# Kernel tuning notes

Measured on AMD Instinct MI355X. Metric: run time of the kernel, lower is better.

Reference implementation:

```python
import jax, jax.numpy as jnp
import numpy as np

N_NODES = 100000
N_EDGES = 1600000
F_IN, H1, H2, N_CLASSES = 512, 64, 32, 16


def setup_inputs() -> dict:
    key = jax.random.key(0)
    ks = jax.random.split(key, 8)
    glorot = lambda k, fi, fo: jax.random.normal(k, (fi, fo), jnp.float32) * (2.0 / (fi + fo)) ** 0.5
    return {
        "x": jax.random.normal(ks[0], (N_NODES, F_IN), jnp.float32),
        "edge_index": jax.random.randint(ks[1], (2, N_EDGES), 0, N_NODES, jnp.int32),
        "W1": glorot(ks[2], F_IN, H1), "b1": jnp.zeros((H1,), jnp.float32),
        "W2": glorot(ks[3], H1, H2), "b2": jnp.zeros((H2,), jnp.float32),
        "W3": glorot(ks[4], H2, N_CLASSES), "b3": jnp.zeros((N_CLASSES,), jnp.float32),
    }


def _gcn_conv(x, W, b, src, dst, norm, n_nodes):
    # GCNConv: D^{-1/2} (A + I) D^{-1/2} X W + b  (transform-then-propagate)
    h = x @ W                                   # [N, out]
    msg = h[src] * norm[:, None]                # gather + scale, [E', out]
    agg = jax.ops.segment_sum(msg, dst, num_segments=n_nodes)  # scatter-add
    return agg + b


def reference(x, edge_index, W1, b1, W2, b2, W3, b3):
    n = x.shape[0]
    loop = jnp.arange(n, dtype=edge_index.dtype)
    src = jnp.concatenate([edge_index[0], loop])  # add self-loops
    dst = jnp.concatenate([edge_index[1], loop])
    deg = jax.ops.segment_sum(jnp.ones_like(src, dtype=x.dtype), dst, num_segments=n)
    dinv = jnp.where(deg > 0, jax.lax.rsqrt(deg), 0.0)
    norm = dinv[src] * dinv[dst]                  # symmetric normalization per edge

    h = jax.nn.relu(_gcn_conv(x, W1, b1, src, dst, norm, n))
    h = jax.nn.relu(_gcn_conv(h, W2, b2, src, dst, norm, n))  # dropout = identity (eval)
    h = _gcn_conv(h, W3, b3, src, dst, norm, n)
    return jax.nn.log_softmax(h, axis=1)
```

## Files before the change

kernel.cpp:

```cpp
#include <hip/hip_runtime.h>
#include <hip/hip_bf16.h>
#include <cstdint>
#include <cstddef>

#define N_NODES 100000
#define N_EDGES 1600000
#define F_IN 512
#define H1F 64
#define H2F 32
#define NCF 16

typedef __attribute__((ext_vector_type(8))) short bf16x8;
typedef __attribute__((ext_vector_type(4))) float f32x4;

__device__ inline short f2bf(float f) {
    uint32_t u = __builtin_bit_cast(uint32_t, f);
    return (short)((u + 0x7FFF + ((u >> 16) & 1)) >> 16);
}

__global__ __launch_bounds__(256) void hist_kernel(const int* __restrict__ dst,
                                                   int* __restrict__ cnt) {
    int e = blockIdx.x * 256 + threadIdx.x;
    if (e < N_EDGES) atomicAdd(&cnt[dst[e]], 1);
}

__global__ __launch_bounds__(512) void scanA_kernel(const int* __restrict__ cnt,
                                                    int* __restrict__ bsums) {
    __shared__ int sh[8];
    int i = blockIdx.x * 512 + threadIdx.x;
    int v = (i < N_NODES) ? cnt[i] : 0;
    #pragma unroll
    for (int o = 32; o > 0; o >>= 1) v += __shfl_down(v, o);
    if ((threadIdx.x & 63) == 0) sh[threadIdx.x >> 6] = v;
    __syncthreads();
    if (threadIdx.x == 0) {
        int t = 0;
        #pragma unroll
        for (int w = 0; w < 8; ++w) t += sh[w];
        bsums[blockIdx.x] = t;
    }
}

__global__ __launch_bounds__(256) void scanB_kernel(int* __restrict__ bsums, int n) {
    __shared__ int s[256];
    int t = threadIdx.x;
    int v = (t < n) ? bsums[t] : 0;
    s[t] = v;
    __syncthreads();
    for (int o = 1; o < 256; o <<= 1) {
        int a = (t >= o) ? s[t - o] : 0;
        __syncthreads();
        s[t] += a;
        __syncthreads();
    }
    if (t < n) bsums[t] = s[t] - v;
}

__global__ __launch_bounds__(512) void scanC_kernel(const int* __restrict__ cnt,
                                                    const int* __restrict__ bsums,
                                                    int* __restrict__ row_ptr,
                                                    int* __restrict__ cursor) {
    __shared__ int s[512];
    int t = threadIdx.x;
    int i = blockIdx.x * 512 + t;
    int v = (i < N_NODES) ? cnt[i] : 0;
    s[t] = v;
    __syncthreads();
    for (int o = 1; o < 512; o <<= 1) {
        int a = (t >= o) ? s[t - o] : 0;
        __syncthreads();
        s[t] += a;
        __syncthreads();
    }
    if (i < N_NODES) {
        int ex = s[t] - v + bsums[blockIdx.x];
        row_ptr[i] = ex;
        cursor[i]  = ex;
    }
    if (i == N_NODES - 1) row_ptr[N_NODES] = s[t] + bsums[blockIdx.x];
}

__global__ __launch_bounds__(256) void dinv_kernel(const int* __restrict__ cnt,
                                                   float* __restrict__ dinv) {
    int i = blockIdx.x * 256 + threadIdx.x;
    if (i < N_NODES) dinv[i] = rsqrtf((float)(cnt[i] + 1));
}

__global__ __launch_bounds__(256) void scatter_kernel(const int* __restrict__ src,
                                                      const int* __restrict__ dst,
                                                      int* __restrict__ cursor,
                                                      int* __restrict__ col) {
    int e = blockIdx.x * 256 + threadIdx.x;
    if (e < N_EDGES) {
        int d = dst[e];
        int pos = atomicAdd(&cursor[d], 1);
        col[pos] = src[e];
    }
}

__global__ __launch_bounds__(256) void gemm1_mfma(const float* __restrict__ x,
                                                  const float* __restrict__ W,
                                                  const float* __restrict__ dinv,
                                                  float* __restrict__ out) {
    __shared__ short As[2][4096];
    __shared__ short Bs[2][2048];
    const int tid = threadIdx.x;
    const int L = tid & 63;
    const int w = tid >> 6;
    const int brow = blockIdx.x * 128;

    f32x4 acc[2][4] = {};

    auto stageA = [&](int kt, int buf) {
        #pragma unroll
        for (int h = 0; h < 2; ++h) {
            int r  = (tid >> 2) + h * 64;
            int kg = tid & 3;
            int gr = brow + r;
            float4 v0 = make_float4(0.f, 0.f, 0.f, 0.f);
            float4 v1 = make_float4(0.f, 0.f, 0.f, 0.f);
            if (gr < N_NODES) {
                const float* p = &x[(size_t)gr * F_IN + kt * 32 + kg * 8];
                v0 = *reinterpret_cast<const float4*>(p);
                v1 = *reinterpret_cast<const float4*>(p + 4);
            }
            short t8[8] = {f2bf(v0.x), f2bf(v0.y), f2bf(v0.z), f2bf(v0.w),
                           f2bf(v1.x), f2bf(v1.y), f2bf(v1.z), f2bf(v1.w)};
            *reinterpret_cast<bf16x8*>(&As[buf][kg * 1024 + (r ^ (kg << 2)) * 8]) =
                *reinterpret_cast<bf16x8*>(t8);
        }
    };
    auto stageB = [&](int kt, int buf) {
        int k0 = kt * 32 + w * 8;
        short t8[8];
        #pragma unroll
        for (int i = 0; i < 8; ++i) t8[i] = f2bf(W[(size_t)(k0 + i) * H1F + L]);
        int byteoff = L * 64 + ((w * 16) ^ ((L & 3) << 4));
        *reinterpret_cast<bf16x8*>((char*)Bs[buf] + byteoff) =
            *reinterpret_cast<bf16x8*>(t8);
    };
    auto compute = [&](int buf) {
        const int kg = L >> 4;
        const int lr = L & 15;
        int r0 = w * 32 + lr;
        int r1 = r0 + 16;
        bf16x8 a0 = *reinterpret_cast<bf16x8*>(&As[buf][kg * 1024 + (r0 ^ (kg << 2)) * 8]);
        bf16x8 a1 = *reinterpret_cast<bf16x8*>(&As[buf][kg * 1024 + (r1 ^ (kg << 2)) * 8]);
        #pragma unroll
        for (int ni = 0; ni < 4; ++ni) {
            int c = ni * 16 + lr;
            bf16x8 b = *reinterpret_cast<bf16x8*>(
                (char*)Bs[buf] + c * 64 + ((kg * 16) ^ ((c & 3) << 4)));
            acc[0][ni] = __builtin_amdgcn_mfma_f32_16x16x32_bf16(a0, b, acc[0][ni], 0, 0, 0);
            acc[1][ni] = __builtin_amdgcn_mfma_f32_16x16x32_bf16(a1, b, acc[1][ni], 0, 0, 0);
        }
    };

    stageA(0, 0);
    stageB(0, 0);
    __syncthreads();
    for (int kt = 0; kt < 16; ++kt) {
        int cur = kt & 1;
        if (kt < 15) {
            stageA(kt + 1, cur ^ 1);
            stageB(kt + 1, cur ^ 1);
        }
        compute(cur);
        __syncthreads();
    }

    #pragma unroll
    for (int mi = 0; mi < 2; ++mi) {
        #pragma unroll
        for (int i = 0; i < 4; ++i) {
            int row = brow + w * 32 + mi * 16 + (L >> 4) * 4 + i;
            if (row < N_NODES) {
                float dv = dinv[row];
                #pragma unroll
                for (int ni = 0; ni < 4; ++ni)
                    out[(size_t)row * H1F + ni * 16 + (L & 15)] = acc[mi][ni][i] * dv;
            }
        }
    }
}

__global__ __launch_bounds__(256) void gemm2_kernel(const float* __restrict__ h,
                                                    const float* __restrict__ W,
                                                    const float* __restrict__ dinv,
                                                    float* __restrict__ out) {
    __shared__ float ws[64][32];
    __shared__ float rs[8][64];
    int tid = threadIdx.x;
    int brow = blockIdx.x * 8;
    #pragma unroll
    for (int i = 0; i < 2; ++i) {
        int f = tid + i * 256;
        reinterpret_cast<float4*>(&ws[0][0])[f] = reinterpret_cast<const float4*>(W)[f];
    }
    if (tid < 128) {
        float4 v = reinterpret_cast<const float4*>(h)[(size_t)brow * 16 + tid];
        reinterpret_cast<float4*>(&rs[0][0])[tid] = v;
    }
    __syncthreads();
    int lr = tid >> 5;
    int c = tid & 31;
    float acc = 0.f;
    #pragma unroll
    for (int k = 0; k < 64; ++k) acc += rs[lr][k] * ws[k][c];
    int gr = brow + lr;
    out[(size_t)gr * H2F + c] = acc * dinv[gr];
}

__global__ __launch_bounds__(256) void gemm3_kernel(const float* __restrict__ h,
                                                    const float* __restrict__ W,
                                                    const float* __restrict__ dinv,
                                                    float* __restrict__ out) {
    __shared__ float ws[32][16];
    __shared__ float rs[16][32];
    int tid = threadIdx.x;
    int brow = blockIdx.x * 16;
    if (tid < 128) {
        reinterpret_cast<float4*>(&ws[0][0])[tid] = reinterpret_cast<const float4*>(W)[tid];
    } else {
        int t = tid - 128;
        float4 v = reinterpret_cast<const float4*>(h)[(size_t)brow * 8 + t];
        reinterpret_cast<float4*>(&rs[0][0])[t] = v;
    }
    __syncthreads();
    int lr = tid >> 4;
    int c = tid & 15;
    float acc = 0.f;
    #pragma unroll
    for (int k = 0; k < 32; ++k) acc += rs[lr][k] * ws[k][c];
    int gr = brow + lr;
    out[(size_t)gr * NCF + c] = acc * dinv[gr];
}

template <int F, bool RELU, bool LSM>
__global__ __launch_bounds__(256) void aggregate_kernel(const float* __restrict__ h,
                                                        const int* __restrict__ row_ptr,
                                                        const int* __restrict__ col,
                                                        const float* __restrict__ dinv,
                                                        const float* __restrict__ bias,
                                                        float* __restrict__ out) {
    int tid = blockIdx.x * 256 + threadIdx.x;
    int n = tid / F;
    int f = tid % F;
    if (n >= N_NODES) return;
    int beg = row_ptr[n];
    int end = row_ptr[n + 1];
    float sum = h[(size_t)n * F + f];
    int j = beg;
    for (; j + 3 < end; j += 4) {
        int c0 = col[j], c1 = col[j + 1], c2 = col[j + 2], c3 = col[j + 3];
        float s0 = h[(size_t)c0 * F + f];
        float s1 = h[(size_t)c1 * F + f];
        float s2 = h[(size_t)c2 * F + f];
        float s3 = h[(size_t)c3 * F + f];
        sum += (s0 + s1) + (s2 + s3);
    }
    for (; j < end; ++j) sum += h[(size_t)col[j] * F + f];

    float val = sum * dinv[n] + bias[f];
    if (RELU) val = fmaxf(val, 0.f);
    if (LSM) {
        float m = val;
        #pragma unroll
        for (int o = 1; o < F; o <<= 1) m = fmaxf(m, __shfl_xor(m, o));
        float ex = expf(val - m);
        float s = ex;
        #pragma unroll
        for (int o = 1; o < F; o <<= 1) s += __shfl_xor(s, o);
        val = val - m - logf(s);
    }
    out[(size_t)n * F + f] = val;
}

extern "C" void kernel_launch(void* const* d_in, const int* in_sizes, int n_in,
                              void* d_out, int out_size, void* d_ws, size_t ws_size,
                              hipStream_t stream) {
    const float* x  = (const float*)d_in[0];
    const int*   ei = (const int*)d_in[1];
    const float* W1 = (const float*)d_in[2];
    const float* b1 = (const float*)d_in[3];
    const float* W2 = (const float*)d_in[4];
    const float* b2 = (const float*)d_in[5];
    const float* W3 = (const float*)d_in[6];
    const float* b3 = (const float*)d_in[7];
    float* out = (float*)d_out;

    const int* src = ei;
    const int* dst = ei + N_EDGES;

    char* ws = (char*)d_ws;
    size_t off = 0;
    auto alloc = [&](size_t bytes) -> void* {
        void* p = ws + off;
        off += (bytes + 255) & ~(size_t)255;
        return p;
    };
    int*   cnt     = (int*)alloc((size_t)N_NODES * 4);
    int*   row_ptr = (int*)alloc((size_t)(N_NODES + 1) * 4);
    int*   cursor  = (int*)alloc((size_t)N_NODES * 4);
    int*   bsums   = (int*)alloc(1024);
    float* dinv    = (float*)alloc((size_t)N_NODES * 4);
    int*   col     = (int*)alloc((size_t)N_EDGES * 4);
    float* bufA    = (float*)alloc((size_t)N_NODES * 64 * 4);
    float* bufB    = (float*)alloc((size_t)N_NODES * 64 * 4);

    const int nChunks = (N_NODES + 511) / 512;

    hipMemsetAsync(cnt, 0, (size_t)N_NODES * 4, stream);
    hist_kernel<<<(N_EDGES + 255) / 256, 256, 0, stream>>>(dst, cnt);
    scanA_kernel<<<nChunks, 512, 0, stream>>>(cnt, bsums);
    scanB_kernel<<<1, 256, 0, stream>>>(bsums, nChunks);
    scanC_kernel<<<nChunks, 512, 0, stream>>>(cnt, bsums, row_ptr, cursor);
    dinv_kernel<<<(N_NODES + 255) / 256, 256, 0, stream>>>(cnt, dinv);
    scatter_kernel<<<(N_EDGES + 255) / 256, 256, 0, stream>>>(src, dst, cursor, col);

    gemm1_mfma<<<(N_NODES + 127) / 128, 256, 0, stream>>>(x, W1, dinv, bufA);
    aggregate_kernel<64, true, false><<<(N_NODES * 64) / 256, 256, 0, stream>>>(
        bufA, row_ptr, col, dinv, b1, bufB);

    gemm2_kernel<<<N_NODES / 8, 256, 0, stream>>>(bufB, W2, dinv, bufA);
    aggregate_kernel<32, true, false><<<(N_NODES * 32) / 256, 256, 0, stream>>>(
        bufA, row_ptr, col, dinv, b2, bufB);

    gemm3_kernel<<<N_NODES / 16, 256, 0, stream>>>(bufB, W3, dinv, bufA);
    aggregate_kernel<16, false, true><<<(N_NODES * 16) / 256, 256, 0, stream>>>(
        bufA, row_ptr, col, dinv, b3, out);
}
```

Baseline: 667.9 us.

## Build CSR via two-level bucketed counting sort with shared-memory histograms

Replaces the per-node global-atomic histogram, three-kernel scan and per-node scatter with a two-level bucketed sort. Edges are first histogrammed and scattered into 782 buckets of 128 destination nodes, with the local node index packed into high bits of the source id. A per-bucket kernel then computes node counts, row_ptr, dinv and the final col ordering using shared-memory atomics. This cuts global atomic contention and the number of launches, at the cost of an extra pass over an intermediate edge buffer that reuses bufA.

```diff
diff --git a/kernel.cpp b/kernel.cpp
--- a/kernel.cpp
+++ b/kernel.cpp
@@ -9,6 +9,7 @@
 #define H1F 64
 #define H2F 32
 #define NCF 16
+#define NB 782
 
 typedef __attribute__((ext_vector_type(8))) short bf16x8;
 typedef __attribute__((ext_vector_type(4))) float f32x4;
@@ -18,83 +19,97 @@
     return (short)((u + 0x7FFF + ((u >> 16) & 1)) >> 16);
 }
 
-__global__ __launch_bounds__(256) void hist_kernel(const int* __restrict__ dst,
-                                                   int* __restrict__ cnt) {
-    int e = blockIdx.x * 256 + threadIdx.x;
-    if (e < N_EDGES) atomicAdd(&cnt[dst[e]], 1);
-}
-
-__global__ __launch_bounds__(512) void scanA_kernel(const int* __restrict__ cnt,
-                                                    int* __restrict__ bsums) {
-    __shared__ int sh[8];
-    int i = blockIdx.x * 512 + threadIdx.x;
-    int v = (i < N_NODES) ? cnt[i] : 0;
-    #pragma unroll
-    for (int o = 32; o > 0; o >>= 1) v += __shfl_down(v, o);
-    if ((threadIdx.x & 63) == 0) sh[threadIdx.x >> 6] = v;
-    __syncthreads();
-    if (threadIdx.x == 0) {
-        int t = 0;
-        #pragma unroll
-        for (int w = 0; w < 8; ++w) t += sh[w];
-        bsums[blockIdx.x] = t;
-    }
-}
-
-__global__ __launch_bounds__(256) void scanB_kernel(int* __restrict__ bsums, int n) {
-    __shared__ int s[256];
+__global__ __launch_bounds__(256) void bhist_kernel(const int* __restrict__ dst,
+                                                    int* __restrict__ bcnt) {
+    __shared__ int lh[NB];
+    for (int i = threadIdx.x; i < NB; i += 256) lh[i] = 0;
+    __syncthreads();
+    for (int e = blockIdx.x * 256 + threadIdx.x; e < N_EDGES; e += 256 * 256)
+        atomicAdd(&lh[dst[e] >> 7], 1);
+    __syncthreads();
+    for (int i = threadIdx.x; i < NB; i += 256) {
+        int v = lh[i];
+        if (v) atomicAdd(&bcnt[i], v);
+    }
+}
+
+__global__ __launch_bounds__(1024) void bscan_kernel(const int* __restrict__ bcnt,
+                                                     int* __restrict__ boff,
+                                                     int* __restrict__ bcur,
+                                                     int* __restrict__ row_ptr) {
+    __shared__ int s[1024];
     int t = threadIdx.x;
-    int v = (t < n) ? bsums[t] : 0;
+    int v = (t < NB) ? bcnt[t] : 0;
     s[t] = v;
     __syncthreads();
-    for (int o = 1; o < 256; o <<= 1) {
+    for (int o = 1; o < 1024; o <<= 1) {
         int a = (t >= o) ? s[t - o] : 0;
         __syncthreads();
         s[t] += a;
         __syncthreads();
     }
-    if (t < n) bsums[t] = s[t] - v;
-}
-
-__global__ __launch_bounds__(512) void scanC_kernel(const int* __restrict__ cnt,
-                                                    const int* __restrict__ bsums,
-                                                    int* __restrict__ row_ptr,
-                                                    int* __restrict__ cursor) {
-    __shared__ int s[512];
-    int t = threadIdx.x;
-    int i = blockIdx.x * 512 + t;
-    int v = (i < N_NODES) ? cnt[i] : 0;
-    s[t] = v;
-    __syncthreads();
-    for (int o = 1; o < 512; o <<= 1) {
-        int a = (t >= o) ? s[t - o] : 0;
-        __syncthreads();
-        s[t] += a;
-        __syncthreads();
-    }
-    if (i < N_NODES) {
-        int ex = s[t] - v + bsums[blockIdx.x];
-        row_ptr[i] = ex;
-        cursor[i]  = ex;
-    }
-    if (i == N_NODES - 1) row_ptr[N_NODES] = s[t] + bsums[blockIdx.x];
-}
-
-__global__ __launch_bounds__(256) void dinv_kernel(const int* __restrict__ cnt,
-                                                   float* __restrict__ dinv) {
-    int i = blockIdx.x * 256 + threadIdx.x;
-    if (i < N_NODES) dinv[i] = rsqrtf((float)(cnt[i] + 1));
-}
-
-__global__ __launch_bounds__(256) void scatter_kernel(const int* __restrict__ src,
-                                                      const int* __restrict__ dst,
-                                                      int* __restrict__ cursor,
-                                                      int* __restrict__ col) {
+    if (t < NB) {
+        int ex = s[t] - v;
+        boff[t] = ex;
+        bcur[t] = ex;
+    }
+    if (t == 0) {
+        boff[NB] = N_EDGES;
+        row_ptr[N_NODES] = N_EDGES;
+    }
+}
+
+__global__ __launch_bounds__(256) void bscatter_kernel(const int* __restrict__ src,
+                                                       const int* __restrict__ dst,
+                                                       int* __restrict__ bcur,
+                                                       int* __restrict__ ebuf) {
     int e = blockIdx.x * 256 + threadIdx.x;
     if (e < N_EDGES) {
         int d = dst[e];
-        int pos = atomicAdd(&cursor[d], 1);
-        col[pos] = src[e];
+        int b = d >> 7;
+        int pos = atomicAdd(&bcur[b], 1);
+        ebuf[pos] = src[e] | ((d & 127) << 17);
+    }
+}
+
+__global__ __launch_bounds__(256) void bbuild_kernel(const int* __restrict__ ebuf,
+                                                     const int* __restrict__ boff,
+                                                     int* __restrict__ row_ptr,
+                                                     int* __restrict__ col,
+                                                     float* __restrict__ dinv) {
+    __shared__ int lcnt[128], lexc[128];
+    int b = blockIdx.x;
+    int beg = boff[b], end = boff[b + 1];
+    int t = threadIdx.x;
+    if (t < 128) lcnt[t] = 0;
+    __syncthreads();
+    for (int j = beg + t; j < end; j += 256)
+        atomicAdd(&lcnt[(ebuf[j] >> 17) & 127], 1);
+    __syncthreads();
+    if (t < 128) lexc[t] = lcnt[t];
+    __syncthreads();
+    for (int o = 1; o < 128; o <<= 1) {
+        int a = (t < 128 && t >= o) ? lexc[t - o] : 0;
+        __syncthreads();
+        if (t < 128) lexc[t] += a;
+        __syncthreads();
+    }
+    int node0 = b << 7;
+    if (t < 128) {
+        int n = node0 + t;
+        if (n < N_NODES) {
+            int ex = lexc[t] - lcnt[t];
+            row_ptr[n] = beg + ex;
+            dinv[n] = rsqrtf((float)(lcnt[t] + 1));
+            lexc[t] = ex;
+        }
+    }
+    __syncthreads();
+    for (int j = beg + t; j < end; j += 256) {
+        int v = ebuf[j];
+        int li = (v >> 17) & 127;
+        int p = atomicAdd(&lexc[li], 1);
+        col[beg + p] = v & 0x1FFFF;
     }
 }
 
@@ -299,24 +314,21 @@
         off += (bytes + 255) & ~(size_t)255;
         return p;
     };
-    int*   cnt     = (int*)alloc((size_t)N_NODES * 4);
     int*   row_ptr = (int*)alloc((size_t)(N_NODES + 1) * 4);
-    int*   cursor  = (int*)alloc((size_t)N_NODES * 4);
-    int*   bsums   = (int*)alloc(1024);
     float* dinv    = (float*)alloc((size_t)N_NODES * 4);
     int*   col     = (int*)alloc((size_t)N_EDGES * 4);
     float* bufA    = (float*)alloc((size_t)N_NODES * 64 * 4);
     float* bufB    = (float*)alloc((size_t)N_NODES * 64 * 4);
-
-    const int nChunks = (N_NODES + 511) / 512;
-
-    hipMemsetAsync(cnt, 0, (size_t)N_NODES * 4, stream);
-    hist_kernel<<<(N_EDGES + 255) / 256, 256, 0, stream>>>(dst, cnt);
-    scanA_kernel<<<nChunks, 512, 0, stream>>>(cnt, bsums);
-    scanB_kernel<<<1, 256, 0, stream>>>(bsums, nChunks);
-    scanC_kernel<<<nChunks, 512, 0, stream>>>(cnt, bsums, row_ptr, cursor);
-    dinv_kernel<<<(N_NODES + 255) / 256, 256, 0, stream>>>(cnt, dinv);
-    scatter_kernel<<<(N_EDGES + 255) / 256, 256, 0, stream>>>(src, dst, cursor, col);
+    int*   bcnt    = (int*)alloc((size_t)NB * 4);
+    int*   boff    = (int*)alloc((size_t)(NB + 1) * 4);
+    int*   bcur    = (int*)alloc((size_t)NB * 4);
+    int*   ebuf    = (int*)bufA;
+
+    hipMemsetAsync(bcnt, 0, (size_t)NB * 4, stream);
+    bhist_kernel<<<256, 256, 0, stream>>>(dst, bcnt);
+    bscan_kernel<<<1, 1024, 0, stream>>>(bcnt, boff, bcur, row_ptr);
+    bscatter_kernel<<<(N_EDGES + 255) / 256, 256, 0, stream>>>(src, dst, bcur, ebuf);
+    bbuild_kernel<<<NB, 256, 0, stream>>>(ebuf, boff, row_ptr, col, dinv);
 
     gemm1_mfma<<<(N_NODES + 127) / 128, 256, 0, stream>>>(x, W1, dinv, bufA);
     aggregate_kernel<64, true, false><<<(N_NODES * 64) / 256, 256, 0, stream>>>(
```

After: 890.2 us. 1.33x slower.
